# Kernel tuning notes

Hardware: AMD Instinct MI355X
Metric: run time of the kernel (lower is better)

Reference implementation:

```python
import jax, jax.numpy as jnp
import numpy as np

# Dimensions
B, T, IN = 8, 64, 6       # batch, timesteps, strain components
G = 256                   # grain_num
H = 32                    # hidden_dim (units)
W = 128                   # quadratic block width
OUT = 3                   # output_dim
DEPTH = 4                 # quadratic block depth
SD = H + IN               # start_dim = units + in_channels = 38
EPS = 1e-15


def setup_inputs() -> dict:
    key = jax.random.key(0)
    ks = jax.random.split(key, 24)
    s = 0.08  # xavier-ish scale for width-128 linears
    d = {
        "x": jax.random.normal(ks[0], (B, T, IN), dtype=jnp.float32),
        "init_ori": jax.random.normal(ks[1], (B, G, 3), dtype=jnp.float32),
        # Quadratic block branch A (modlist1): first layer SD->W, then (DEPTH-1) W->W
        "qbA_W0": jax.random.normal(ks[2], (SD, W)) * s,
        "qbA_b0": jnp.zeros((W,), jnp.float32),
        "qbA_Ws": jax.random.normal(ks[3], (DEPTH - 1, W, W)) * s,
        "qbA_bs": jnp.zeros((DEPTH - 1, W), jnp.float32),
        # Quadratic block branch B (modlist2)
        "qbB_W0": jax.random.normal(ks[4], (SD, W)) * s,
        "qbB_b0": jnp.zeros((W,), jnp.float32),
        "qbB_Ws": jax.random.normal(ks[5], (DEPTH - 1, W, W)) * s,
        "qbB_bs": jnp.zeros((DEPTH - 1, W), jnp.float32),
        # fc_alpha: W -> H ; fc_beta (1-layer DNN): W -> H
        "alpha_W": jax.random.normal(ks[6], (W, H)) * s,
        "alpha_b": jnp.zeros((H,), jnp.float32),
        "beta_W": jax.random.normal(ks[7], (W, H)) * s,
        "beta_b": jnp.zeros((H,), jnp.float32),
        # nn_out DNN: layers = [H, 128, 128, OUT], tanh between hidden layers
        "out_W0": jax.random.normal(ks[8], (H, 128)) * s,
        "out_b0": jnp.zeros((128,), jnp.float32),
        "out_W1": jax.random.normal(ks[9], (128, 128)) * s,
        "out_b1": jnp.zeros((128,), jnp.float32),
        "out_W2": jax.random.normal(ks[10], (128, OUT)) * s,
        "out_b2": jnp.zeros((OUT,), jnp.float32),
    }
    return d


def reference(x, init_ori, qbA_W0, qbA_b0, qbA_Ws, qbA_bs,
              qbB_W0, qbB_b0, qbB_Ws, qbB_bs,
              alpha_W, alpha_b, beta_W, beta_b,
              out_W0, out_b0, out_W1, out_b1, out_W2, out_b2):
    b = x.shape[0]
    # h0 = zeros with first 3 hidden channels set to initial orientations
    h0 = jnp.zeros((b, G, H), x.dtype).at[:, :, :3].set(init_ori)

    def step(h, x_t):  # h: [B,G,H], x_t: [B,IN]
        sn = jnp.linalg.norm(x_t, axis=-1, keepdims=True)          # [B,1]
        xn = x_t / (sn + EPS)                                      # normalized strain direction
        z = jnp.concatenate(
            [jnp.broadcast_to(xn[:, None, :], (b, G, IN)), h], axis=-1)  # [B,G,SD]
        # quadratic block: elementwise product of two linear branches
        a = jnp.tanh(z @ qbA_W0 + qbA_b0)
        c = jnp.tanh(z @ qbB_W0 + qbB_b0)
        z = a * c
        for j in range(DEPTH - 1):
            a = z @ qbA_Ws[j] + qbA_bs[j]
            c = z @ qbB_Ws[j] + qbB_bs[j]
            if j < DEPTH - 2:  # tanh on all but the last quadratic layer
                a = jnp.tanh(a)
                c = jnp.tanh(c)
            z = a * c
        q = jnp.tanh(z)                                            # [B,G,W]
        alpha = jnp.exp(q @ alpha_W + alpha_b)                     # [B,G,H]
        beta = jnp.tanh(q @ beta_W + beta_b)                       # [B,G,H]
        decay = jnp.exp(-alpha * sn[:, :, None])                   # exp(-alpha*||strain||)
        h_new = decay * (h - beta) + beta                          # gated state update
        # nn_out DNN [H,128,128,OUT] with tanh hidden activations
        o = jnp.tanh(h_new @ out_W0 + out_b0)
        o = jnp.tanh(o @ out_W1 + out_b1)
        o = o @ out_W2 + out_b2                                    # [B,G,OUT]
        return h_new, o

    _, outs = jax.lax.scan(step, h0, jnp.swapaxes(x, 0, 1))        # outs: [T,B,G,OUT]
    return jnp.transpose(outs, (1, 2, 0, 3))                       # [B,G,T,OUT]
```

## Files before the change

### kernel.cpp

```cpp
#include <hip/hip_runtime.h>

typedef _Float16 f16;
typedef _Float16 f16x4 __attribute__((ext_vector_type(4)));
typedef _Float16 f16x8 __attribute__((ext_vector_type(8)));
typedef float f32x4 __attribute__((ext_vector_type(4)));
typedef unsigned int u32;

#define MFMA16(a,b,c) __builtin_amdgcn_mfma_f32_16x16x32_f16(a,b,c,0,0,0)

#define BAR() asm volatile("s_waitcnt lgkmcnt(0)\n\ts_barrier" ::: "memory")

#define OFF_A0 0
#define OFF_B0 8192
#define OFF_AW 16384
#define OFF_BW 65536
#define OFF_AL 114688
#define OFF_BE 118784
#define OFF_O0 122880
#define OFF_O1 126976
#define OFF_O2 143360
#define PACK_TOTAL 145408
#define OFF_HH 262144

struct PackSrcs { const float* p[9]; };

__global__ __launch_bounds__(256) void pack_all(PackSrcs ps, f16* __restrict__ dst){
  int idx = blockIdx.x*256 + threadIdx.x;
  if (idx >= PACK_TOTAL) return;
  const float* src; int base, Kreal, Nreal, KT;
  if (idx < 16384){
    if (idx < 8192){ src=ps.p[0]; base=0; } else { src=ps.p[1]; base=8192; }
    Kreal=38; Nreal=128; KT=2;
  } else if (idx < 65536){
    int s=(idx-16384)>>14; src=ps.p[2]+s*16384; base=16384+s*16384; Kreal=128; Nreal=128; KT=4;
  } else if (idx < 114688){
    int s=(idx-65536)>>14; src=ps.p[3]+s*16384; base=65536+s*16384; Kreal=128; Nreal=128; KT=4;
  } else if (idx < 122880){
    if (idx<118784){ src=ps.p[4]; base=114688; } else { src=ps.p[5]; base=118784; }
    Kreal=128; Nreal=32; KT=4;
  } else if (idx < 126976){
    src=ps.p[6]; base=122880; Kreal=32; Nreal=128; KT=1;
  } else if (idx < 143360){
    src=ps.p[7]; base=126976; Kreal=128; Nreal=128; KT=4;
  } else {
    src=ps.p[8]; base=143360; Kreal=128; Nreal=3; KT=4;
  }
  int local = idx - base;
  int j = local & 7, lane = (local>>3)&63, rem = local>>9;
  int kt = rem % KT, nt = rem / KT;
  int k = kt*32 + ((lane>>4)<<3) + j;
  int n = nt*16 + (lane&15);
  if (base < 16384) k = (k < 32) ? (k + 6) : 99;
  dst[idx] = (f16)((k<Kreal && n<Nreal) ? src[k*Nreal+n] : 0.f);
}

__device__ __forceinline__ float tanhfast(float x){
  float e = __builtin_amdgcn_exp2f(x * 2.885390082f);
  return 1.f - 2.f*__builtin_amdgcn_rcpf(e + 1.f);
}
__device__ __forceinline__ float expfast(float x){
  return __builtin_amdgcn_exp2f(x * 1.44269504f);
}

__device__ __forceinline__ f16x8 ldW(const f16* wp, int off, int KT, int nt, int kt, int l){
  return *(const f16x8*)(wp + off + (((nt*KT + kt)*64 + l)<<3));
}

template<int LAST>
__device__ __forceinline__ void qphase(const f16* __restrict__ Zi, f16* __restrict__ Zo,
                                       const f16x8 (&WA)[4], const f16x8 (&WB)[4],
                                       f32x4 bA4, f32x4 bB4,
                                       int l, int d0, int n16){
  f16x8 Bq[4];
#pragma unroll
  for (int kt=0; kt<4; ++kt) Bq[kt] = *(const f16x8*)(Zi + ((kt*64 + l)<<3));
  f32x4 a = bA4;
  f32x4 c = bB4;
#pragma unroll
  for (int kt=0; kt<4; ++kt){
    a = MFMA16(WA[kt], Bq[kt], a);
    c = MFMA16(WB[kt], Bq[kt], c);
  }
  f16x4 z4;
#pragma unroll
  for (int i=0;i<4;++i){
    float z = LAST ? tanhfast(a[i]*c[i]) : tanhfast(a[i])*tanhfast(c[i]);
    z4[i] = (f16)z;
  }
  int kt_o = d0>>5, lane_o = (((d0&31)>>3)<<4) | n16, j0 = d0&7;
  *(f16x4*)(Zo + ((kt_o*64 + lane_o)<<3) + j0) = z4;
}

__global__ __launch_bounds__(512,2)
void lmsc_rec(const float* __restrict__ x, const float* __restrict__ init_ori,
              const f16* __restrict__ wp,
              const float* __restrict__ w0Araw, const float* __restrict__ w0Braw,
              const float* __restrict__ ba0, const float* __restrict__ bas,
              const float* __restrict__ bb0, const float* __restrict__ bbs,
              const float* __restrict__ b_al, const float* __restrict__ b_be,
              f16* __restrict__ hG)
{
  __shared__ __align__(16) f16 S[2][512];
  __shared__ __align__(16) f16 Z[2][2048];
  __shared__ float xnL[64][8];
  __shared__ __align__(16) float UA[64][128];
  __shared__ __align__(16) float UC[64][128];

  const int tid = (int)threadIdx.x;
  const int l = tid & 63, wid = tid >> 6;
  const int n16 = l & 15, rhi = l >> 4;
  const int d0 = (wid<<4) + (rhi<<2);
  const int tile = (int)blockIdx.x, b = tile >> 4, Rbase = tile << 4;

  f16x8 w0A = ldW(wp, OFF_A0, 2, wid, 0, l);
  f16x8 w0B = ldW(wp, OFF_B0, 2, wid, 0, l);
  f16x8 wqA[3][4], wqB[3][4];
#pragma unroll
  for (int ly=0;ly<3;++ly)
#pragma unroll
    for (int kt=0;kt<4;++kt){
      wqA[ly][kt] = ldW(wp, OFF_AW + ly*16384, 4, wid, kt, l);
      wqB[ly][kt] = ldW(wp, OFF_BW + ly*16384, 4, wid, kt, l);
    }
  f32x4 bA_r[3], bB_r[3];
#pragma unroll
  for (int ly=0;ly<3;++ly){
    bA_r[ly] = *(const f32x4*)(bas + ly*128 + d0);
    bB_r[ly] = *(const f32x4*)(bbs + ly*128 + d0);
  }
  const int d0p = (wid<<4) + (rhi<<2);
  f16x8 wal[4], wbe[4];
  f32x4 uaB = {0,0,0,0}, ubB = {0,0,0,0};
  if (wid < 2){
#pragma unroll
    for (int kt=0;kt<4;++kt){
      wal[kt] = ldW(wp, OFF_AL, 4, wid, kt, l);
      wbe[kt] = ldW(wp, OFF_BE, 4, wid, kt, l);
    }
    uaB = *(const f32x4*)(b_al + d0p);
    ubB = *(const f32x4*)(b_be + d0p);
  }

  if (tid < 64){
    const float* xp = x + (b*64 + tid)*6;
    float s2 = 0.f;
#pragma unroll
    for (int i=0;i<6;++i) s2 += xp[i]*xp[i];
    float sn = sqrtf(s2);
    float inv = 1.f/(sn + 1e-15f);
#pragma unroll
    for (int i=0;i<6;++i) xnL[tid][i] = xp[i]*inv;
    xnL[tid][6] = sn;
  }
  float hreg[4] = {0.f,0.f,0.f,0.f};
  if (wid < 2){
#pragma unroll
    for (int i=0;i<4;++i){
      int c = d0p + i;
      hreg[i] = (c < 3) ? init_ori[(Rbase + n16)*3 + c] : 0.f;
    }
  }
  __syncthreads();
  {
    const int dim = tid & 127, t0 = (tid >> 7) << 4;
    float wA[6], wC[6];
#pragma unroll
    for (int k=0;k<6;++k){ wA[k] = w0Araw[k*128+dim]; wC[k] = w0Braw[k*128+dim]; }
    const float bA_ = ba0[dim], bC_ = bb0[dim];
#pragma unroll
    for (int tt=0;tt<16;++tt){
      int t = t0 + tt;
      float aA = bA_, aC = bC_;
#pragma unroll
      for (int k=0;k<6;++k){
        float xv = xnL[t][k];
        aA += xv * wA[k];
        aC += xv * wC[k];
      }
      UA[t][dim] = aA; UC[t][dim] = aC;
    }
  }
  if (tid < 256){
    int r = tid & 15, cc = tid >> 4;
#pragma unroll
    for (int e=0;e<2;++e){
      int c = cc + e*16;
      float h0 = (c < 3) ? init_ori[(Rbase + r)*3 + c] : 0.f;
      f16 hh = (f16)h0, hl = (f16)(h0 - (float)hh);
      int idx = ((((c>>3)<<4) | r)<<3) + (c&7);
      S[0][idx] = hh; S[1][idx] = hl;
    }
  }
  __syncthreads();

  for (int t=0; t<64; ++t){
    {
      f16x8 Bh = *(const f16x8*)(&S[0][l<<3]);
      f16x8 Bl = *(const f16x8*)(&S[1][l<<3]);
      f32x4 aH = *(const f32x4*)(&UA[t][d0]);
      f32x4 cH = *(const f32x4*)(&UC[t][d0]);
      f32x4 aL = {0,0,0,0}, cL = {0,0,0,0};
      aH = MFMA16(w0A, Bh, aH); aL = MFMA16(w0A, Bl, aL);
      cH = MFMA16(w0B, Bh, cH); cL = MFMA16(w0B, Bl, cL);
      f16x4 z4;
#pragma unroll
      for (int i=0;i<4;++i)
        z4[i] = (f16)(tanhfast(aH[i]+aL[i]) * tanhfast(cH[i]+cL[i]));
      int kt_o = d0>>5, lane_o = (((d0&31)>>3)<<4) | n16, j0 = d0&7;
      *(f16x4*)(&Z[0][((kt_o*64 + lane_o)<<3) + j0]) = z4;
    }
    BAR();
    qphase<0>(Z[0], Z[1], wqA[0], wqB[0], bA_r[0], bB_r[0], l, d0, n16);
    BAR();
    qphase<0>(Z[1], Z[0], wqA[1], wqB[1], bA_r[1], bB_r[1], l, d0, n16);
    BAR();
    qphase<1>(Z[0], Z[1], wqA[2], wqB[2], bA_r[2], bB_r[2], l, d0, n16);
    BAR();
    if (wid < 2){
      f16x8 q[4];
#pragma unroll
      for (int kt=0;kt<4;++kt) q[kt] = *(const f16x8*)(&Z[1][(kt*64+l)<<3]);
      f32x4 ua = uaB;
      f32x4 ub = ubB;
#pragma unroll
      for (int kt=0;kt<4;++kt){
        ua = MFMA16(wal[kt], q[kt], ua);
        ub = MFMA16(wbe[kt], q[kt], ub);
      }
      float sn = xnL[t][6];
      int mt = tile*64 + t;
      f16x4 hh4, hl4;
#pragma unroll
      for (int i=0;i<4;++i){
        float alv = expfast(fminf(ua[i], 80.f));
        float bev = tanhfast(ub[i]);
        float hn = __builtin_amdgcn_exp2f(-1.44269504f*alv*sn)*(hreg[i] - bev) + bev;
        hreg[i] = hn;
        f16 hh = (f16)hn; hh4[i] = hh; hl4[i] = (f16)(hn - (float)hh);
      }
      if (t < 63){
        int sb = ((((d0p>>3)<<4) | n16)<<3) + (d0p&7);
        *(f16x4*)(&S[0][sb]) = hh4;
        *(f16x4*)(&S[1][sb]) = hl4;
      }
      int lane_o = ((d0p>>3)<<4) | n16;
      *(f16x4*)(hG + mt*512 + lane_o*8 + (d0p&7)) = hh4;
    }
    BAR();
  }
}

__global__ __launch_bounds__(512,4)
void lmsc_out(const f16* __restrict__ wp, const f16* __restrict__ hG,
              const float* __restrict__ bo0, const float* __restrict__ bo1,
              const float* __restrict__ bo2, float* __restrict__ out)
{
  __shared__ __align__(16) f16 o1b[16384];
  __shared__ __align__(16) f16 o2b[16384];
  const int tid=(int)threadIdx.x, l=tid&63, wid=tid>>6;
  const int n16=l&15, rhi=l>>4;
  const int mtb = (int)blockIdx.x * 8;
  f16x8 W0a = ldW(wp, OFF_O0, 1, wid, 0, l);
  f16x8 W1a[4], W2a[4];
#pragma unroll
  for (int kt=0;kt<4;++kt){ W1a[kt]=ldW(wp,OFF_O1,4,wid,kt,l); W2a[kt]=ldW(wp,OFF_O2,4,0,kt,l); }
  const int d0 = wid*16 + rhi*4;
  const f32x4 b0v = *(const f32x4*)(bo0 + d0);
  const f32x4 b1v = *(const f32x4*)(bo1 + d0);
  const int kt_o = d0>>5, lane_o = (((d0&31)>>3)<<4) + n16, j0 = d0&7;
#pragma unroll
  for (int s=0;s<8;++s){
    int mt = mtb + s;
    f16x8 Bh = *(const f16x8*)(hG + ((mt*64+l)<<3));
    f32x4 acc = b0v;
    acc = MFMA16(W0a, Bh, acc);
    f16x4 z4;
#pragma unroll
    for (int i=0;i<4;++i) z4[i] = (f16)tanhfast(acc[i]);
    *(f16x4*)(&o1b[(((s*4+kt_o)*64 + lane_o)<<3) + j0]) = z4;
  }
  __syncthreads();
#pragma unroll
  for (int s=0;s<8;++s){
    f32x4 acc = b1v;
#pragma unroll
    for (int kt=0;kt<4;++kt){
      f16x8 B = *(const f16x8*)(&o1b[((s*4+kt)*64 + l)<<3]);
      acc = MFMA16(W1a[kt], B, acc);
    }
    f16x4 z4;
#pragma unroll
    for (int i=0;i<4;++i) z4[i] = (f16)tanhfast(acc[i]);
    *(f16x4*)(&o2b[(((s*4+kt_o)*64 + lane_o)<<3) + j0]) = z4;
  }
  __syncthreads();
  {
    f32x4 acc = {0,0,0,0};
#pragma unroll
    for (int kt=0;kt<4;++kt){
      f16x8 B = *(const f16x8*)(&o2b[((wid*4+kt)*64 + l)<<3]);
      acc = MFMA16(W2a[kt], B, acc);
    }
    if (l < 16){
      int mt = mtb + wid, grow = (mt>>6)*16 + n16, tt = mt & 63;
#pragma unroll
      for (int i=0;i<3;++i)
        out[(grow*64 + tt)*3 + i] = acc[i] + bo2[i];
    }
  }
}

extern "C" void kernel_launch(void* const* d_in, const int* in_sizes, int n_in,
                              void* d_out, int out_size, void* d_ws, size_t ws_size,
                              hipStream_t stream){
  const float* x        = (const float*)d_in[0];
  const float* init_ori = (const float*)d_in[1];
  f16* wp = (f16*)d_ws;

  PackSrcs ps;
  ps.p[0] = (const float*)d_in[2];
  ps.p[1] = (const float*)d_in[6];
  ps.p[2] = (const float*)d_in[4];
  ps.p[3] = (const float*)d_in[8];
  ps.p[4] = (const float*)d_in[10];
  ps.p[5] = (const float*)d_in[12];
  ps.p[6] = (const float*)d_in[14];
  ps.p[7] = (const float*)d_in[16];
  ps.p[8] = (const float*)d_in[18];
  pack_all<<<(PACK_TOTAL+255)/256, 256, 0, stream>>>(ps, wp);

  lmsc_rec<<<128,512,0,stream>>>(x, init_ori, wp,
      (const float*)d_in[2],  (const float*)d_in[6],
      (const float*)d_in[3],  (const float*)d_in[5],
      (const float*)d_in[7],  (const float*)d_in[9],
      (const float*)d_in[11], (const float*)d_in[13],
      wp + OFF_HH);
  lmsc_out<<<1024,512,0,stream>>>(wp, wp + OFF_HH,
      (const float*)d_in[15], (const float*)d_in[17], (const float*)d_in[19],
      (float*)d_out);
}
```

Measured before the change: 131.9 us.

## Fuse output MLP into recurrent kernel as pipelined stages on idle waves

```diff
diff --git a/kernel.cpp b/kernel.cpp
--- a/kernel.cpp
+++ b/kernel.cpp
@@ -20,7 +20,6 @@
 #define OFF_O1 126976
 #define OFF_O2 143360
 #define PACK_TOTAL 145408
-#define OFF_HH 262144
 
 struct PackSrcs { const float* p[9]; };
 
@@ -98,10 +97,13 @@
               const float* __restrict__ ba0, const float* __restrict__ bas,
               const float* __restrict__ bb0, const float* __restrict__ bbs,
               const float* __restrict__ b_al, const float* __restrict__ b_be,
-              f16* __restrict__ hG)
+              const float* __restrict__ bo0, const float* __restrict__ bo1,
+              const float* __restrict__ bo2, float* __restrict__ out)
 {
-  __shared__ __align__(16) f16 S[2][512];
+  __shared__ __align__(16) f16 S[2][2][512];
   __shared__ __align__(16) f16 Z[2][2048];
+  __shared__ __align__(16) f16 o1buf[2][2048];
+  __shared__ __align__(16) f16 o2buf[2][2048];
   __shared__ float xnL[64][8];
   __shared__ __align__(16) float UA[64][128];
   __shared__ __align__(16) float UC[64][128];
@@ -140,6 +142,31 @@
     uaB = *(const f32x4*)(b_al + d0p);
     ubB = *(const f32x4*)(b_be + d0p);
   }
+  f16x8 wo1[4][4]; f32x4 bo1r[4];
+  if (wid == 2 || wid == 3){
+#pragma unroll
+    for (int j=0;j<4;++j){
+      int nt = (wid-2)*4 + j;
+#pragma unroll
+      for (int kt=0;kt<4;++kt) wo1[j][kt] = ldW(wp, OFF_O1, 4, nt, kt, l);
+      bo1r[j] = *(const f32x4*)(bo1 + nt*16 + (rhi<<2));
+    }
+  }
+  f16x8 wo0[4]; f32x4 bo0r[4];
+  if (wid == 4 || wid == 5){
+#pragma unroll
+    for (int j=0;j<4;++j){
+      int nt = (wid-4)*4 + j;
+      wo0[j] = ldW(wp, OFF_O0, 1, nt, 0, l);
+      bo0r[j] = *(const f32x4*)(bo0 + nt*16 + (rhi<<2));
+    }
+  }
+  f16x8 wo2[4]; float b2r0=0.f, b2r1=0.f, b2r2=0.f;
+  if (wid == 6){
+#pragma unroll
+    for (int kt=0;kt<4;++kt) wo2[kt] = ldW(wp, OFF_O2, 4, 0, kt, l);
+    b2r0 = bo2[0]; b2r1 = bo2[1]; b2r2 = bo2[2];
+  }
 
   if (tid < 64){
     const float* xp = x + (b*64 + tid)*6;
@@ -188,35 +215,37 @@
       float h0 = (c < 3) ? init_ori[(Rbase + r)*3 + c] : 0.f;
       f16 hh = (f16)h0, hl = (f16)(h0 - (float)hh);
       int idx = ((((c>>3)<<4) | r)<<3) + (c&7);
-      S[0][idx] = hh; S[1][idx] = hl;
+      S[0][0][idx] = hh; S[0][1][idx] = hl;
     }
   }
   __syncthreads();
 
-  for (int t=0; t<64; ++t){
-    {
-      f16x8 Bh = *(const f16x8*)(&S[0][l<<3]);
-      f16x8 Bl = *(const f16x8*)(&S[1][l<<3]);
-      f32x4 aH = *(const f32x4*)(&UA[t][d0]);
-      f32x4 cH = *(const f32x4*)(&UC[t][d0]);
-      f32x4 aL = {0,0,0,0}, cL = {0,0,0,0};
-      aH = MFMA16(w0A, Bh, aH); aL = MFMA16(w0A, Bl, aL);
-      cH = MFMA16(w0B, Bh, cH); cL = MFMA16(w0B, Bl, cL);
-      f16x4 z4;
-#pragma unroll
-      for (int i=0;i<4;++i)
-        z4[i] = (f16)(tanhfast(aH[i]+aL[i]) * tanhfast(cH[i]+cL[i]));
-      int kt_o = d0>>5, lane_o = (((d0&31)>>3)<<4) | n16, j0 = d0&7;
-      *(f16x4*)(&Z[0][((kt_o*64 + lane_o)<<3) + j0]) = z4;
-    }
-    BAR();
-    qphase<0>(Z[0], Z[1], wqA[0], wqB[0], bA_r[0], bB_r[0], l, d0, n16);
-    BAR();
-    qphase<0>(Z[1], Z[0], wqA[1], wqB[1], bA_r[1], bB_r[1], l, d0, n16);
-    BAR();
-    qphase<1>(Z[0], Z[1], wqA[2], wqB[2], bA_r[2], bB_r[2], l, d0, n16);
-    BAR();
-    if (wid < 2){
+  for (int t=0; t<67; ++t){
+    if (t < 64){
+      {
+        f16x8 Bh = *(const f16x8*)(&S[t&1][0][l<<3]);
+        f16x8 Bl = *(const f16x8*)(&S[t&1][1][l<<3]);
+        f32x4 aH = *(const f32x4*)(&UA[t][d0]);
+        f32x4 cH = *(const f32x4*)(&UC[t][d0]);
+        f32x4 aL = {0,0,0,0}, cL = {0,0,0,0};
+        aH = MFMA16(w0A, Bh, aH); aL = MFMA16(w0A, Bl, aL);
+        cH = MFMA16(w0B, Bh, cH); cL = MFMA16(w0B, Bl, cL);
+        f16x4 z4;
+#pragma unroll
+        for (int i=0;i<4;++i)
+          z4[i] = (f16)(tanhfast(aH[i]+aL[i]) * tanhfast(cH[i]+cL[i]));
+        int kt_o = d0>>5, lane_o = (((d0&31)>>3)<<4) | n16, j0 = d0&7;
+        *(f16x4*)(&Z[0][((kt_o*64 + lane_o)<<3) + j0]) = z4;
+      }
+      BAR();
+      qphase<0>(Z[0], Z[1], wqA[0], wqB[0], bA_r[0], bB_r[0], l, d0, n16);
+      BAR();
+      qphase<0>(Z[1], Z[0], wqA[1], wqB[1], bA_r[1], bB_r[1], l, d0, n16);
+      BAR();
+      qphase<1>(Z[0], Z[1], wqA[2], wqB[2], bA_r[2], bB_r[2], l, d0, n16);
+      BAR();
+    }
+    if (t < 64 && wid < 2){
       f16x8 q[4];
 #pragma unroll
       for (int kt=0;kt<4;++kt) q[kt] = *(const f16x8*)(&Z[1][(kt*64+l)<<3]);
@@ -228,7 +257,6 @@
         ub = MFMA16(wbe[kt], q[kt], ub);
       }
       float sn = xnL[t][6];
-      int mt = tile*64 + t;
       f16x4 hh4, hl4;
 #pragma unroll
       for (int i=0;i<4;++i){
@@ -238,75 +266,59 @@
         hreg[i] = hn;
         f16 hh = (f16)hn; hh4[i] = hh; hl4[i] = (f16)(hn - (float)hh);
       }
-      if (t < 63){
-        int sb = ((((d0p>>3)<<4) | n16)<<3) + (d0p&7);
-        *(f16x4*)(&S[0][sb]) = hh4;
-        *(f16x4*)(&S[1][sb]) = hl4;
-      }
-      int lane_o = ((d0p>>3)<<4) | n16;
-      *(f16x4*)(hG + mt*512 + lane_o*8 + (d0p&7)) = hh4;
+      int sb = ((((d0p>>3)<<4) | n16)<<3) + (d0p&7);
+      *(f16x4*)(&S[(t+1)&1][0][sb]) = hh4;
+      *(f16x4*)(&S[(t+1)&1][1][sb]) = hl4;
+    }
+    if ((wid == 4 || wid == 5) && t >= 1 && t <= 64){
+      f16x8 Bh = *(const f16x8*)(&S[t&1][0][l<<3]);
+      f16* o1w = &o1buf[(t+1)&1][0];
+#pragma unroll
+      for (int j=0;j<4;++j){
+        f32x4 acc = bo0r[j];
+        acc = MFMA16(wo0[j], Bh, acc);
+        f16x4 z4;
+#pragma unroll
+        for (int i=0;i<4;++i) z4[i] = (f16)tanhfast(acc[i]);
+        int d0s = ((wid-4)*4 + j)*16 + (rhi<<2);
+        int kt_o = d0s>>5, lane_o = (((d0s&31)>>3)<<4) | n16, j0 = d0s&7;
+        *(f16x4*)(o1w + ((kt_o*64 + lane_o)<<3) + j0) = z4;
+      }
+    }
+    if ((wid == 2 || wid == 3) && t >= 2 && t <= 65){
+      f16x8 Bq[4];
+#pragma unroll
+      for (int kt=0;kt<4;++kt) Bq[kt] = *(const f16x8*)(&o1buf[t&1][(kt*64+l)<<3]);
+      f16* o2w = &o2buf[t&1][0];
+#pragma unroll
+      for (int j=0;j<4;++j){
+        f32x4 acc = bo1r[j];
+#pragma unroll
+        for (int kt=0;kt<4;++kt) acc = MFMA16(wo1[j][kt], Bq[kt], acc);
+        f16x4 z4;
+#pragma unroll
+        for (int i=0;i<4;++i) z4[i] = (f16)tanhfast(acc[i]);
+        int d0s = ((wid-2)*4 + j)*16 + (rhi<<2);
+        int kt_o = d0s>>5, lane_o = (((d0s&31)>>3)<<4) | n16, j0 = d0s&7;
+        *(f16x4*)(o2w + ((kt_o*64 + lane_o)<<3) + j0) = z4;
+      }
+    }
+    if (wid == 6 && t >= 3){
+      f16x8 Bq[4];
+#pragma unroll
+      for (int kt=0;kt<4;++kt) Bq[kt] = *(const f16x8*)(&o2buf[(t+1)&1][(kt*64+l)<<3]);
+      f32x4 acc = {0,0,0,0};
+#pragma unroll
+      for (int kt=0;kt<4;++kt) acc = MFMA16(wo2[kt], Bq[kt], acc);
+      if (l < 16){
+        int t3 = t - 3;
+        float* op = out + ((Rbase + l)*64 + t3)*3;
+        op[0] = acc[0] + b2r0;
+        op[1] = acc[1] + b2r1;
+        op[2] = acc[2] + b2r2;
+      }
     }
     BAR();
-  }
-}
-
-__global__ __launch_bounds__(512,4)
-void lmsc_out(const f16* __restrict__ wp, const f16* __restrict__ hG,
-              const float* __restrict__ bo0, const float* __restrict__ bo1,
-              const float* __restrict__ bo2, float* __restrict__ out)
-{
-  __shared__ __align__(16) f16 o1b[16384];
-  __shared__ __align__(16) f16 o2b[16384];
-  const int tid=(int)threadIdx.x, l=tid&63, wid=tid>>6;
-  const int n16=l&15, rhi=l>>4;
-  const int mtb = (int)blockIdx.x * 8;
-  f16x8 W0a = ldW(wp, OFF_O0, 1, wid, 0, l);
-  f16x8 W1a[4], W2a[4];
-#pragma unroll
-  for (int kt=0;kt<4;++kt){ W1a[kt]=ldW(wp,OFF_O1,4,wid,kt,l); W2a[kt]=ldW(wp,OFF_O2,4,0,kt,l); }
-  const int d0 = wid*16 + rhi*4;
-  const f32x4 b0v = *(const f32x4*)(bo0 + d0);
-  const f32x4 b1v = *(const f32x4*)(bo1 + d0);
-  const int kt_o = d0>>5, lane_o = (((d0&31)>>3)<<4) + n16, j0 = d0&7;
-#pragma unroll
-  for (int s=0;s<8;++s){
-    int mt = mtb + s;
-    f16x8 Bh = *(const f16x8*)(hG + ((mt*64+l)<<3));
-    f32x4 acc = b0v;
-    acc = MFMA16(W0a, Bh, acc);
-    f16x4 z4;
-#pragma unroll
-    for (int i=0;i<4;++i) z4[i] = (f16)tanhfast(acc[i]);
-    *(f16x4*)(&o1b[(((s*4+kt_o)*64 + lane_o)<<3) + j0]) = z4;
-  }
-  __syncthreads();
-#pragma unroll
-  for (int s=0;s<8;++s){
-    f32x4 acc = b1v;
-#pragma unroll
-    for (int kt=0;kt<4;++kt){
-      f16x8 B = *(const f16x8*)(&o1b[((s*4+kt)*64 + l)<<3]);
-      acc = MFMA16(W1a[kt], B, acc);
-    }
-    f16x4 z4;
-#pragma unroll
-    for (int i=0;i<4;++i) z4[i] = (f16)tanhfast(acc[i]);
-    *(f16x4*)(&o2b[(((s*4+kt_o)*64 + lane_o)<<3) + j0]) = z4;
-  }
-  __syncthreads();
-  {
-    f32x4 acc = {0,0,0,0};
-#pragma unroll
-    for (int kt=0;kt<4;++kt){
-      f16x8 B = *(const f16x8*)(&o2b[((wid*4+kt)*64 + l)<<3]);
-      acc = MFMA16(W2a[kt], B, acc);
-    }
-    if (l < 16){
-      int mt = mtb + wid, grow = (mt>>6)*16 + n16, tt = mt & 63;
-#pragma unroll
-      for (int i=0;i<3;++i)
-        out[(grow*64 + tt)*3 + i] = acc[i] + bo2[i];
-    }
   }
 }
 
@@ -334,8 +346,6 @@
       (const float*)d_in[3],  (const float*)d_in[5],
       (const float*)d_in[7],  (const float*)d_in[9],
       (const float*)d_in[11], (const float*)d_in[13],
-      wp + OFF_HH);
-  lmsc_out<<<1024,512,0,stream>>>(wp, wp + OFF_HH,
       (const float*)d_in[15], (const float*)d_in[17], (const float*)d_in[19],
       (float*)d_out);
 }
```

After: 268.2 us. +103.2%, slower.
